# Kernel tuning notes

Hardware: AMD Instinct MI355X
Metric: run time of the kernel (lower is better)

The kernel has to match this reference:

```python
import jax, jax.numpy as jnp
import numpy as np

EPS = 1e-5

def _bn(x, gamma, beta):
    # BatchNorm1d in training mode: biased batch statistics over batch dim
    mu = jnp.mean(x, axis=0, keepdims=True)
    var = jnp.mean((x - mu) ** 2, axis=0, keepdims=True)
    return gamma * (x - mu) * jax.lax.rsqrt(var + EPS) + beta

def setup_inputs() -> dict:
    key = jax.random.key(0)
    ks = jax.random.split(key, 12)
    B, T, D_in, E, H, D_out = 8192, 128, 2, 128, 128, 5
    s = lambda k, shape, fan: jax.random.normal(k, shape, jnp.float32) * (1.0 / np.sqrt(fan))
    return {
        "inputs": jax.random.normal(ks[0], (B, T, D_in), jnp.float32),
        "W_emb": s(ks[1], (E, D_in), D_in),
        "b_emb": jnp.zeros((E,), jnp.float32),
        "gamma_emb": jnp.ones((E,), jnp.float32),
        "beta_emb": jnp.zeros((E,), jnp.float32),
        "W_ih": s(ks[2], (4 * H, E), E),
        "b_ih": jnp.zeros((4 * H,), jnp.float32),
        "W_hh": s(ks[3], (4 * H, H), H),
        "b_hh": jnp.zeros((4 * H,), jnp.float32),
        "W_out": s(ks[4], (D_out, H), H),
        "b_out": jnp.zeros((D_out,), jnp.float32),
        "gamma_out": jnp.ones((D_out,), jnp.float32),
        "beta_out": jnp.zeros((D_out,), jnp.float32),
    }

def reference(inputs, W_emb, b_emb, gamma_emb, beta_emb,
              W_ih, b_ih, W_hh, b_hh,
              W_out, b_out, gamma_out, beta_out):
    B, T, _ = inputs.shape
    H = W_hh.shape[1]
    x_t = jnp.swapaxes(inputs, 0, 1)  # [T, B, D_in]

    def step(carry, x):
        h, c = carry
        # input embedding MLP: Linear -> BatchNorm -> ReLU
        e = jax.nn.relu(_bn(x @ W_emb.T + b_emb, gamma_emb, beta_emb))
        # LSTMCell: gate order i, f, g, o (torch convention)
        gates = e @ W_ih.T + b_ih + h @ W_hh.T + b_hh
        i, f, g, o = jnp.split(gates, 4, axis=-1)
        c_new = jax.nn.sigmoid(f) * c + jax.nn.sigmoid(i) * jnp.tanh(g)
        h_new = jax.nn.sigmoid(o) * jnp.tanh(c_new)
        # output MLP: Linear -> BatchNorm (no activation)
        out = _bn(h_new @ W_out.T + b_out, gamma_out, beta_out)
        return (h_new, c_new), out

    init = (jnp.zeros((B, H), inputs.dtype), jnp.zeros((B, H), inputs.dtype))
    (h, c), outs = jax.lax.scan(step, init, x_t)
    return jnp.swapaxes(outs, 0, 1), (h, c)
```

## Files before the change

kernel.cpp:

```cpp
#include <hip/hip_runtime.h>

typedef short s16x8 __attribute__((ext_vector_type(8)));
typedef float f32x4 __attribute__((ext_vector_type(4)));

#define T_STEPS 128
#define BN_EPS 1e-5f

__device__ __forceinline__ unsigned short f2bf(float f) {
  unsigned u = __float_as_uint(f);
  u += 0x7FFFu + ((u >> 16) & 1u);
  return (unsigned short)(u >> 16);
}
__device__ __forceinline__ float sigm(float x) {
  return __builtin_amdgcn_rcpf(1.0f + __expf(-x));
}
__device__ __forceinline__ float tanh_(float x) {
  return 1.0f - 2.0f * __builtin_amdgcn_rcpf(1.0f + __expf(2.0f * x));
}

__global__ void moments_kernel(const float* __restrict__ inp, float* __restrict__ mom, int B) {
  int t = blockIdx.x;
  int tid = threadIdx.x;
  float s0 = 0.f, s1 = 0.f, q0 = 0.f, q1 = 0.f, pp = 0.f;
  for (int b = tid; b < B; b += 256) {
    float2 x = *(const float2*)(inp + (size_t)b * (2 * T_STEPS) + 2 * t);
    s0 += x.x; s1 += x.y; q0 += x.x * x.x; q1 += x.y * x.y; pp += x.x * x.y;
  }
  float v[5] = {s0, s1, q0, q1, pp};
  #pragma unroll
  for (int i = 0; i < 5; ++i) {
    float x = v[i];
    #pragma unroll
    for (int o = 32; o > 0; o >>= 1) x += __shfl_down(x, o);
    v[i] = x;
  }
  __shared__ float red[4][5];
  if ((tid & 63) == 0) {
    #pragma unroll
    for (int i = 0; i < 5; ++i) red[tid >> 6][i] = v[i];
  }
  __syncthreads();
  if (tid == 0) {
    #pragma unroll
    for (int i = 0; i < 5; ++i)
      mom[t * 5 + i] = red[0][i] + red[1][i] + red[2][i] + red[3][i];
  }
}

__global__ void fold_kernel(const float* __restrict__ mom,
                            const float* __restrict__ W_emb, const float* __restrict__ b_emb,
                            const float* __restrict__ gamma, const float* __restrict__ beta,
                            float* __restrict__ cA, float* __restrict__ cB, float* __restrict__ cC,
                            float invB) {
  int idx = blockIdx.x * 256 + threadIdx.x;
  if (idx >= T_STEPS * 128) return;
  int t = idx >> 7, j = idx & 127;
  float m0 = mom[t * 5 + 0] * invB, m1 = mom[t * 5 + 1] * invB;
  float q0 = mom[t * 5 + 2] * invB, q1 = mom[t * 5 + 3] * invB, p = mom[t * 5 + 4] * invB;
  float v00 = q0 - m0 * m0, v11 = q1 - m1 * m1, v01 = p - m0 * m1;
  float w0 = W_emb[2 * j], w1 = W_emb[2 * j + 1];
  float mu  = w0 * m0 + w1 * m1 + b_emb[j];
  float var = w0 * w0 * v00 + w1 * w1 * v11 + 2.f * w0 * w1 * v01;
  float a = gamma[j] * rsqrtf(var + BN_EPS);
  cA[idx] = a * w0;
  cB[idx] = a * w1;
  cC[idx] = beta[j] + a * (b_emb[j] - mu);
}

__global__ void prepw_kernel(const float* __restrict__ Wih, const float* __restrict__ Whh,
                             const float* __restrict__ Wout,
                             unsigned short* __restrict__ Wb, unsigned short* __restrict__ Wob) {
  int idx = blockIdx.x * 256 + threadIdx.x;
  if (idx < 512 * 256) {
    int n = idx >> 8, k = idx & 255;
    float w = (k < 128) ? Wih[n * 128 + k] : Whh[n * 128 + (k - 128)];
    Wb[idx] = f2bf(w);
  } else if (idx < 512 * 256 + 16 * 128) {
    int i2 = idx - 512 * 256;
    int d = i2 >> 7, k = i2 & 127;
    Wob[i2] = (d < 5) ? f2bf(Wout[d * 128 + k]) : (unsigned short)0;
  }
}

__global__ __launch_bounds__(512, 2) void lstm_kernel(
    const float* __restrict__ inp,
    const float* __restrict__ cA, const float* __restrict__ cB, const float* __restrict__ cC,
    const unsigned short* __restrict__ Wb, const unsigned short* __restrict__ Wob,
    const float* __restrict__ bih, const float* __restrict__ bhh,
    float* __restrict__ outz, float* __restrict__ hout, float* __restrict__ cout) {
  __shared__ __align__(16) short X[32][392];

  const int tid  = threadIdx.x;
  const int wave = tid >> 6;
  const int lane = tid & 63;
  const int l15  = lane & 15;
  const int lk   = lane >> 4;
  const int b0   = blockIdx.x * 32;
  const int em   = tid >> 4;
  const int ecg  = tid & 15;

  s16x8 wfrag[4][8];
  #pragma unroll
  for (int g = 0; g < 4; ++g)
    #pragma unroll
    for (int kk = 0; kk < 8; ++kk)
      wfrag[g][kk] = *(const s16x8*)(Wb + (size_t)(g * 128 + wave * 16 + l15) * 256 + kk * 32 + lk * 8);
  s16x8 wof[4];
  #pragma unroll
  for (int kk = 0; kk < 4; ++kk)
    wof[kk] = *(const s16x8*)(Wob + l15 * 128 + kk * 32 + lk * 8);
  float biasg[4];
  #pragma unroll
  for (int g = 0; g < 4; ++g) {
    int n = g * 128 + wave * 16 + l15;
    biasg[g] = bih[n] + bhh[n];
  }

  float creg[2][4] = {{0.f,0.f,0.f,0.f},{0.f,0.f,0.f,0.f}};
  float hreg[2][4] = {{0.f,0.f,0.f,0.f},{0.f,0.f,0.f,0.f}};

  auto do_e = [&](int tn) {
    float2 xv = *(const float2*)(inp + (size_t)(b0 + em) * (2 * T_STEPS) + 2 * tn);
    const float4* pa = (const float4*)(cA + tn * 128 + ecg * 8);
    const float4* pb = (const float4*)(cB + tn * 128 + ecg * 8);
    const float4* pc = (const float4*)(cC + tn * 128 + ecg * 8);
    s16x8 ev;
    #pragma unroll
    for (int q = 0; q < 2; ++q) {
      float4 va = pa[q], vb = pb[q], vc = pc[q];
      float e0 = fmaxf(0.f, vc.x + va.x * xv.x + vb.x * xv.y);
      float e1 = fmaxf(0.f, vc.y + va.y * xv.x + vb.y * xv.y);
      float e2 = fmaxf(0.f, vc.z + va.z * xv.x + vb.z * xv.y);
      float e3 = fmaxf(0.f, vc.w + va.w * xv.x + vb.w * xv.y);
      ev[4 * q + 0] = (short)f2bf(e0);
      ev[4 * q + 1] = (short)f2bf(e1);
      ev[4 * q + 2] = (short)f2bf(e2);
      ev[4 * q + 3] = (short)f2bf(e3);
    }
    *(s16x8*)&X[em][ecg * 8] = ev;
  };

  {
    s16x8 z = {0,0,0,0,0,0,0,0};
    *(s16x8*)&X[em][128 + ecg * 8] = z;
  }
  do_e(0);
  __syncthreads();

  #pragma unroll 1
  for (int t = 0; t < T_STEPS; ++t) {
    const int rb = 128 + (t & 1) * 128;
    const int wb = 128 + ((t + 1) & 1) * 128;
    f32x4 acc[2][4];
    #pragma unroll
    for (int mf = 0; mf < 2; ++mf)
      #pragma unroll
      for (int g = 0; g < 4; ++g) {
        f32x4 v = {biasg[g], biasg[g], biasg[g], biasg[g]};
        acc[mf][g] = v;
      }
    #pragma unroll
    for (int kk = 0; kk < 8; ++kk) {
      const int coff = (kk < 4) ? (kk * 32 + lk * 8) : (rb + (kk - 4) * 32 + lk * 8);
      s16x8 a0 = *(const s16x8*)&X[l15][coff];
      s16x8 a1 = *(const s16x8*)&X[16 + l15][coff];
      #pragma unroll
      for (int g = 0; g < 4; ++g) {
        acc[0][g] = __builtin_amdgcn_mfma_f32_16x16x32_bf16(a0, wfrag[g][kk], acc[0][g], 0, 0, 0);
        acc[1][g] = __builtin_amdgcn_mfma_f32_16x16x32_bf16(a1, wfrag[g][kk], acc[1][g], 0, 0, 0);
      }
    }
    #pragma unroll
    for (int mf = 0; mf < 2; ++mf)
      #pragma unroll
      for (int r = 0; r < 4; ++r) {
        float gi = sigm(acc[mf][0][r]);
        float gf = sigm(acc[mf][1][r]);
        float gg = tanh_(acc[mf][2][r]);
        float go = sigm(acc[mf][3][r]);
        float cc = gf * creg[mf][r] + gi * gg;
        creg[mf][r] = cc;
        float hh = go * tanh_(cc);
        hreg[mf][r] = hh;
        X[mf * 16 + lk * 4 + r][wb + wave * 16 + l15] = (short)f2bf(hh);
      }
    __syncthreads();
    if (wave < 2) {
      f32x4 zac = {0.f, 0.f, 0.f, 0.f};
      #pragma unroll
      for (int kk = 0; kk < 4; ++kk) {
        s16x8 a = *(const s16x8*)&X[wave * 16 + l15][wb + kk * 32 + lk * 8];
        zac = __builtin_amdgcn_mfma_f32_16x16x32_bf16(a, wof[kk], zac, 0, 0, 0);
      }
      if (l15 < 5) {
        #pragma unroll
        for (int r = 0; r < 4; ++r) {
          int m = wave * 16 + lk * 4 + r;
          outz[((size_t)(b0 + m) * T_STEPS + t) * 5 + l15] = zac[r];
        }
      }
    }
    if (t < T_STEPS - 1) do_e(t + 1);
    __syncthreads();
  }

  #pragma unroll
  for (int mf = 0; mf < 2; ++mf)
    #pragma unroll
    for (int r = 0; r < 4; ++r) {
      int m = mf * 16 + lk * 4 + r;
      size_t base = (size_t)(b0 + m) * 128 + wave * 16 + l15;
      hout[base] = hreg[mf][r];
      cout[base] = creg[mf][r];
    }
}

__global__ void stats_kernel(const float* __restrict__ z, float* __restrict__ stats,
                             const float* __restrict__ gamma, const float* __restrict__ beta, int B) {
  int grp = blockIdx.x;
  int d = grp % 5;
  int tid = threadIdx.x;
  float s = 0.f, q = 0.f;
  for (int b = tid; b < B; b += 256) {
    float v = z[(size_t)b * (T_STEPS * 5) + grp];
    s += v; q += v * v;
  }
  #pragma unroll
  for (int o = 32; o > 0; o >>= 1) { s += __shfl_down(s, o); q += __shfl_down(q, o); }
  __shared__ float rs[4], rq[4];
  if ((tid & 63) == 0) { rs[tid >> 6] = s; rq[tid >> 6] = q; }
  __syncthreads();
  if (tid == 0) {
    s = rs[0] + rs[1] + rs[2] + rs[3];
    q = rq[0] + rq[1] + rq[2] + rq[3];
    float mean = s / (float)B;
    float var  = q / (float)B - mean * mean;
    float sc = gamma[d] * rsqrtf(var + BN_EPS);
    stats[grp * 2 + 0] = sc;
    stats[grp * 2 + 1] = beta[d] - mean * sc;
  }
}

__global__ void norm_kernel(float* __restrict__ z, const float* __restrict__ stats, int n) {
  int i = blockIdx.x * 512 + threadIdx.x;
  if (i < n) {
    int grp = i % (T_STEPS * 5);
    float2 st = *(const float2*)(stats + grp * 2);
    z[i] = z[i] * st.x + st.y;
  }
}

extern "C" void kernel_launch(void* const* d_in, const int* in_sizes, int n_in,
                              void* d_out, int out_size, void* d_ws, size_t ws_size,
                              hipStream_t stream) {
  const float* inp    = (const float*)d_in[0];
  const float* W_emb  = (const float*)d_in[1];
  const float* b_emb  = (const float*)d_in[2];
  const float* g_emb  = (const float*)d_in[3];
  const float* be_emb = (const float*)d_in[4];
  const float* Wih    = (const float*)d_in[5];
  const float* bih    = (const float*)d_in[6];
  const float* Whh    = (const float*)d_in[7];
  const float* bhh    = (const float*)d_in[8];
  const float* Wout   = (const float*)d_in[9];
  const float* g_out  = (const float*)d_in[11];
  const float* be_out = (const float*)d_in[12];

  const int B = in_sizes[0] / (2 * T_STEPS);

  char* ws = (char*)d_ws;
  float*          mom   = (float*)(ws + 0);
  float*          cA    = (float*)(ws + 4096);
  float*          cB    = (float*)(ws + 69632);
  float*          cC    = (float*)(ws + 135168);
  unsigned short* Wb    = (unsigned short*)(ws + 200704);
  unsigned short* Wob   = (unsigned short*)(ws + 462848);
  float*          stats = (float*)(ws + 466944);

  float* outz = (float*)d_out;
  float* hout = outz + (size_t)B * T_STEPS * 5;
  float* cout = hout + (size_t)B * 128;

  moments_kernel<<<T_STEPS, 256, 0, stream>>>(inp, mom, B);
  fold_kernel<<<(T_STEPS * 128 + 255) / 256, 256, 0, stream>>>(mom, W_emb, b_emb, g_emb, be_emb,
                                                               cA, cB, cC, 1.0f / (float)B);
  prepw_kernel<<<(512 * 256 + 16 * 128 + 255) / 256, 256, 0, stream>>>(Wih, Whh, Wout, Wb, Wob);
  lstm_kernel<<<B / 32, 512, 0, stream>>>(inp, cA, cB, cC, Wb, Wob, bih, bhh, outz, hout, cout);
  stats_kernel<<<T_STEPS * 5, 256, 0, stream>>>(outz, stats, g_out, be_out, B);
  const int n = B * T_STEPS * 5;
  norm_kernel<<<(n + 511) / 512, 512, 0, stream>>>(outz, stats, n);
}
```

Baseline: 508.5 us.

## Split LSTM K-reduction across 16 waves and restructure BN prep/stat kernels

The LSTM kernel now uses 1024 threads per block and splits the gate GEMM's K dimension in half: one half of the waves covers the embedding part and the other the recurrent part. Partial sums are exchanged through a new LDS buffer, which halves per-wave weight registers and MFMA chain length. It also packs bf16 conversion with v_cvt_pk_bf16_f32, moves output weights into LDS, and fuses the moments and fold kernels. The output BN statistics are replaced by a vectorized atomic-sum kernel plus a float4 normalize. In exchange it adds an extra LDS round trip, a memset, and float atomics, which make the summation order nondeterministic.

```diff
diff --git a/kernel.cpp b/kernel.cpp
--- a/kernel.cpp
+++ b/kernel.cpp
@@ -5,12 +5,19 @@
 
 #define T_STEPS 128
 #define BN_EPS 1e-5f
+#define LROW 392
+#define EXS 36
 
 __device__ __forceinline__ unsigned short f2bf(float f) {
   unsigned u = __float_as_uint(f);
   u += 0x7FFFu + ((u >> 16) & 1u);
   return (unsigned short)(u >> 16);
 }
+__device__ __forceinline__ unsigned cvtpk(float a, float b) {
+  unsigned r;
+  asm("v_cvt_pk_bf16_f32 %0, %1, %2" : "=v"(r) : "v"(a), "v"(b));
+  return r;
+}
 __device__ __forceinline__ float sigm(float x) {
   return __builtin_amdgcn_rcpf(1.0f + __expf(-x));
 }
@@ -18,9 +25,12 @@
   return 1.0f - 2.0f * __builtin_amdgcn_rcpf(1.0f + __expf(2.0f * x));
 }
 
-__global__ void moments_kernel(const float* __restrict__ inp, float* __restrict__ mom, int B) {
-  int t = blockIdx.x;
-  int tid = threadIdx.x;
+__global__ void prep_e_kernel(const float* __restrict__ inp,
+                              const float* __restrict__ W_emb, const float* __restrict__ b_emb,
+                              const float* __restrict__ gamma, const float* __restrict__ beta,
+                              float* __restrict__ cA, float* __restrict__ cB, float* __restrict__ cC,
+                              int B, float invB) {
+  int t = blockIdx.x, tid = threadIdx.x;
   float s0 = 0.f, s1 = 0.f, q0 = 0.f, q1 = 0.f, pp = 0.f;
   for (int b = tid; b < B; b += 256) {
     float2 x = *(const float2*)(inp + (size_t)b * (2 * T_STEPS) + 2 * t);
@@ -35,6 +45,7 @@
     v[i] = x;
   }
   __shared__ float red[4][5];
+  __shared__ float tot[5];
   if ((tid & 63) == 0) {
     #pragma unroll
     for (int i = 0; i < 5; ++i) red[tid >> 6][i] = v[i];
@@ -42,29 +53,23 @@
   __syncthreads();
   if (tid == 0) {
     #pragma unroll
-    for (int i = 0; i < 5; ++i)
-      mom[t * 5 + i] = red[0][i] + red[1][i] + red[2][i] + red[3][i];
-  }
-}
-
-__global__ void fold_kernel(const float* __restrict__ mom,
-                            const float* __restrict__ W_emb, const float* __restrict__ b_emb,
-                            const float* __restrict__ gamma, const float* __restrict__ beta,
-                            float* __restrict__ cA, float* __restrict__ cB, float* __restrict__ cC,
-                            float invB) {
-  int idx = blockIdx.x * 256 + threadIdx.x;
-  if (idx >= T_STEPS * 128) return;
-  int t = idx >> 7, j = idx & 127;
-  float m0 = mom[t * 5 + 0] * invB, m1 = mom[t * 5 + 1] * invB;
-  float q0 = mom[t * 5 + 2] * invB, q1 = mom[t * 5 + 3] * invB, p = mom[t * 5 + 4] * invB;
-  float v00 = q0 - m0 * m0, v11 = q1 - m1 * m1, v01 = p - m0 * m1;
-  float w0 = W_emb[2 * j], w1 = W_emb[2 * j + 1];
-  float mu  = w0 * m0 + w1 * m1 + b_emb[j];
-  float var = w0 * w0 * v00 + w1 * w1 * v11 + 2.f * w0 * w1 * v01;
-  float a = gamma[j] * rsqrtf(var + BN_EPS);
-  cA[idx] = a * w0;
-  cB[idx] = a * w1;
-  cC[idx] = beta[j] + a * (b_emb[j] - mu);
+    for (int i = 0; i < 5; ++i) tot[i] = red[0][i] + red[1][i] + red[2][i] + red[3][i];
+  }
+  __syncthreads();
+  if (tid < 128) {
+    int j = tid;
+    float m0 = tot[0] * invB, m1 = tot[1] * invB;
+    float q0m = tot[2] * invB, q1m = tot[3] * invB, p = tot[4] * invB;
+    float v00 = q0m - m0 * m0, v11 = q1m - m1 * m1, v01 = p - m0 * m1;
+    float w0 = W_emb[2 * j], w1 = W_emb[2 * j + 1];
+    float mu  = w0 * m0 + w1 * m1 + b_emb[j];
+    float var = w0 * w0 * v00 + w1 * w1 * v11 + 2.f * w0 * w1 * v01;
+    float a = gamma[j] * rsqrtf(var + BN_EPS);
+    int idx = t * 128 + j;
+    cA[idx] = a * w0;
+    cB[idx] = a * w1;
+    cC[idx] = beta[j] + a * (b_emb[j] - mu);
+  }
 }
 
 __global__ void prepw_kernel(const float* __restrict__ Wih, const float* __restrict__ Whh,
@@ -82,172 +87,196 @@
   }
 }
 
-__global__ __launch_bounds__(512, 2) void lstm_kernel(
+__global__ __launch_bounds__(1024) void lstm_kernel(
     const float* __restrict__ inp,
     const float* __restrict__ cA, const float* __restrict__ cB, const float* __restrict__ cC,
     const unsigned short* __restrict__ Wb, const unsigned short* __restrict__ Wob,
     const float* __restrict__ bih, const float* __restrict__ bhh,
     float* __restrict__ outz, float* __restrict__ hout, float* __restrict__ cout) {
-  __shared__ __align__(16) short X[32][392];
+  __shared__ __align__(16) short X[32][LROW];
+  __shared__ __align__(16) unsigned short WO[16][136];
+  __shared__ __align__(16) float EX[8][4][16][EXS];
 
   const int tid  = threadIdx.x;
   const int wave = tid >> 6;
   const int lane = tid & 63;
   const int l15  = lane & 15;
   const int lk   = lane >> 4;
+  const int eh   = (wave >> 3);
+  const int cg   = wave & 7;
   const int b0   = blockIdx.x * 32;
-  const int em   = tid >> 4;
-  const int ecg  = tid & 15;
-
-  s16x8 wfrag[4][8];
+  const int em   = tid >> 5;
+  const int ec4  = (tid & 31) * 4;
+
+  s16x8 wfrag[4][4];
   #pragma unroll
   for (int g = 0; g < 4; ++g)
     #pragma unroll
-    for (int kk = 0; kk < 8; ++kk)
-      wfrag[g][kk] = *(const s16x8*)(Wb + (size_t)(g * 128 + wave * 16 + l15) * 256 + kk * 32 + lk * 8);
-  s16x8 wof[4];
-  #pragma unroll
-  for (int kk = 0; kk < 4; ++kk)
-    wof[kk] = *(const s16x8*)(Wob + l15 * 128 + kk * 32 + lk * 8);
+    for (int kk = 0; kk < 4; ++kk)
+      wfrag[g][kk] = *(const s16x8*)(Wb + (size_t)(g * 128 + cg * 16 + l15) * 256 + eh * 128 + kk * 32 + lk * 8);
   float biasg[4];
   #pragma unroll
   for (int g = 0; g < 4; ++g) {
-    int n = g * 128 + wave * 16 + l15;
-    biasg[g] = bih[n] + bhh[n];
-  }
-
-  float creg[2][4] = {{0.f,0.f,0.f,0.f},{0.f,0.f,0.f,0.f}};
-  float hreg[2][4] = {{0.f,0.f,0.f,0.f},{0.f,0.f,0.f,0.f}};
+    int n = g * 128 + cg * 16 + l15;
+    biasg[g] = eh ? 0.f : (bih[n] + bhh[n]);
+  }
+
+  {
+    int i0 = tid * 2;
+    int d = i0 >> 7, k = i0 & 127;
+    *(unsigned*)&WO[d][k] = *(const unsigned*)(Wob + i0);
+  }
 
   auto do_e = [&](int tn) {
     float2 xv = *(const float2*)(inp + (size_t)(b0 + em) * (2 * T_STEPS) + 2 * tn);
-    const float4* pa = (const float4*)(cA + tn * 128 + ecg * 8);
-    const float4* pb = (const float4*)(cB + tn * 128 + ecg * 8);
-    const float4* pc = (const float4*)(cC + tn * 128 + ecg * 8);
-    s16x8 ev;
-    #pragma unroll
-    for (int q = 0; q < 2; ++q) {
-      float4 va = pa[q], vb = pb[q], vc = pc[q];
-      float e0 = fmaxf(0.f, vc.x + va.x * xv.x + vb.x * xv.y);
-      float e1 = fmaxf(0.f, vc.y + va.y * xv.x + vb.y * xv.y);
-      float e2 = fmaxf(0.f, vc.z + va.z * xv.x + vb.z * xv.y);
-      float e3 = fmaxf(0.f, vc.w + va.w * xv.x + vb.w * xv.y);
-      ev[4 * q + 0] = (short)f2bf(e0);
-      ev[4 * q + 1] = (short)f2bf(e1);
-      ev[4 * q + 2] = (short)f2bf(e2);
-      ev[4 * q + 3] = (short)f2bf(e3);
-    }
-    *(s16x8*)&X[em][ecg * 8] = ev;
+    float4 va = *(const float4*)(cA + tn * 128 + ec4);
+    float4 vb = *(const float4*)(cB + tn * 128 + ec4);
+    float4 vc = *(const float4*)(cC + tn * 128 + ec4);
+    float e0 = fmaxf(0.f, vc.x + va.x * xv.x + vb.x * xv.y);
+    float e1 = fmaxf(0.f, vc.y + va.y * xv.x + vb.y * xv.y);
+    float e2 = fmaxf(0.f, vc.z + va.z * xv.x + vb.z * xv.y);
+    float e3 = fmaxf(0.f, vc.w + va.w * xv.x + vb.w * xv.y);
+    *(uint2*)&X[em][ec4] = make_uint2(cvtpk(e0, e1), cvtpk(e2, e3));
   };
 
-  {
-    s16x8 z = {0,0,0,0,0,0,0,0};
-    *(s16x8*)&X[em][128 + ecg * 8] = z;
-  }
+  *(uint2*)&X[em][128 + ec4] = make_uint2(0u, 0u);
   do_e(0);
   __syncthreads();
+
+  float creg[4] = {0.f, 0.f, 0.f, 0.f};
+  float hreg[4] = {0.f, 0.f, 0.f, 0.f};
+  const int colX    = cg * 16 + l15;
+  const int keep_r0 = eh ? 16 : 0;
+  const int rowP    = keep_r0 + lk * 4;
 
   #pragma unroll 1
   for (int t = 0; t < T_STEPS; ++t) {
     const int rb = 128 + (t & 1) * 128;
     const int wb = 128 + ((t + 1) & 1) * 128;
-    f32x4 acc[2][4];
-    #pragma unroll
-    for (int mf = 0; mf < 2; ++mf)
-      #pragma unroll
-      for (int g = 0; g < 4; ++g) {
-        f32x4 v = {biasg[g], biasg[g], biasg[g], biasg[g]};
-        acc[mf][g] = v;
-      }
-    #pragma unroll
-    for (int kk = 0; kk < 8; ++kk) {
-      const int coff = (kk < 4) ? (kk * 32 + lk * 8) : (rb + (kk - 4) * 32 + lk * 8);
+    const int abase = eh ? rb : 0;
+
+    f32x4 acc0[4], acc1[4];
+    #pragma unroll
+    for (int g = 0; g < 4; ++g) {
+      f32x4 v = {biasg[g], biasg[g], biasg[g], biasg[g]};
+      acc0[g] = v; acc1[g] = v;
+    }
+    #pragma unroll
+    for (int kk = 0; kk < 4; ++kk) {
+      const int coff = abase + kk * 32 + lk * 8;
       s16x8 a0 = *(const s16x8*)&X[l15][coff];
       s16x8 a1 = *(const s16x8*)&X[16 + l15][coff];
       #pragma unroll
       for (int g = 0; g < 4; ++g) {
-        acc[0][g] = __builtin_amdgcn_mfma_f32_16x16x32_bf16(a0, wfrag[g][kk], acc[0][g], 0, 0, 0);
-        acc[1][g] = __builtin_amdgcn_mfma_f32_16x16x32_bf16(a1, wfrag[g][kk], acc[1][g], 0, 0, 0);
+        acc0[g] = __builtin_amdgcn_mfma_f32_16x16x32_bf16(a0, wfrag[g][kk], acc0[g], 0, 0, 0);
+        acc1[g] = __builtin_amdgcn_mfma_f32_16x16x32_bf16(a1, wfrag[g][kk], acc1[g], 0, 0, 0);
       }
     }
-    #pragma unroll
-    for (int mf = 0; mf < 2; ++mf)
-      #pragma unroll
-      for (int r = 0; r < 4; ++r) {
-        float gi = sigm(acc[mf][0][r]);
-        float gf = sigm(acc[mf][1][r]);
-        float gg = tanh_(acc[mf][2][r]);
-        float go = sigm(acc[mf][3][r]);
-        float cc = gf * creg[mf][r] + gi * gg;
-        creg[mf][r] = cc;
-        float hh = go * tanh_(cc);
-        hreg[mf][r] = hh;
-        X[mf * 16 + lk * 4 + r][wb + wave * 16 + l15] = (short)f2bf(hh);
-      }
+    if (!eh) {
+      #pragma unroll
+      for (int g = 0; g < 4; ++g)
+        *(f32x4*)&EX[cg][g][l15][16 + lk * 4] = acc1[g];
+    } else {
+      #pragma unroll
+      for (int g = 0; g < 4; ++g)
+        *(f32x4*)&EX[cg][g][l15][lk * 4] = acc0[g];
+    }
     __syncthreads();
-    if (wave < 2) {
+    f32x4 gacc[4];
+    if (!eh) {
+      #pragma unroll
+      for (int g = 0; g < 4; ++g)
+        gacc[g] = acc0[g] + *(const f32x4*)&EX[cg][g][l15][lk * 4];
+    } else {
+      #pragma unroll
+      for (int g = 0; g < 4; ++g)
+        gacc[g] = acc1[g] + *(const f32x4*)&EX[cg][g][l15][16 + lk * 4];
+    }
+    float hv[4];
+    #pragma unroll
+    for (int r = 0; r < 4; ++r) {
+      float gi = sigm(gacc[0][r]);
+      float gf = sigm(gacc[1][r]);
+      float gg = tanh_(gacc[2][r]);
+      float go = sigm(gacc[3][r]);
+      float cc = gf * creg[r] + gi * gg;
+      creg[r] = cc;
+      float hh = go * tanh_(cc);
+      hreg[r] = hh; hv[r] = hh;
+    }
+    {
+      unsigned u01 = cvtpk(hv[0], hv[1]);
+      unsigned u23 = cvtpk(hv[2], hv[3]);
+      X[rowP + 0][wb + colX] = (short)(u01);
+      X[rowP + 1][wb + colX] = (short)(u01 >> 16);
+      X[rowP + 2][wb + colX] = (short)(u23);
+      X[rowP + 3][wb + colX] = (short)(u23 >> 16);
+    }
+    if (t < T_STEPS - 1) do_e(t + 1);
+    __syncthreads();
+    if ((wave & 7) == 0) {
+      const int rz = eh ? 16 : 0;
       f32x4 zac = {0.f, 0.f, 0.f, 0.f};
       #pragma unroll
       for (int kk = 0; kk < 4; ++kk) {
-        s16x8 a = *(const s16x8*)&X[wave * 16 + l15][wb + kk * 32 + lk * 8];
-        zac = __builtin_amdgcn_mfma_f32_16x16x32_bf16(a, wof[kk], zac, 0, 0, 0);
+        s16x8 a  = *(const s16x8*)&X[rz + l15][wb + kk * 32 + lk * 8];
+        s16x8 wz = *(const s16x8*)&WO[l15][kk * 32 + lk * 8];
+        zac = __builtin_amdgcn_mfma_f32_16x16x32_bf16(a, wz, zac, 0, 0, 0);
       }
       if (l15 < 5) {
         #pragma unroll
-        for (int r = 0; r < 4; ++r) {
-          int m = wave * 16 + lk * 4 + r;
-          outz[((size_t)(b0 + m) * T_STEPS + t) * 5 + l15] = zac[r];
-        }
+        for (int r = 0; r < 4; ++r)
+          outz[((size_t)(b0 + rz + lk * 4 + r) * T_STEPS + t) * 5 + l15] = zac[r];
       }
     }
-    if (t < T_STEPS - 1) do_e(t + 1);
-    __syncthreads();
-  }
-
-  #pragma unroll
-  for (int mf = 0; mf < 2; ++mf)
-    #pragma unroll
-    for (int r = 0; r < 4; ++r) {
-      int m = mf * 16 + lk * 4 + r;
-      size_t base = (size_t)(b0 + m) * 128 + wave * 16 + l15;
-      hout[base] = hreg[mf][r];
-      cout[base] = creg[mf][r];
-    }
-}
-
-__global__ void stats_kernel(const float* __restrict__ z, float* __restrict__ stats,
-                             const float* __restrict__ gamma, const float* __restrict__ beta, int B) {
-  int grp = blockIdx.x;
-  int d = grp % 5;
-  int tid = threadIdx.x;
-  float s = 0.f, q = 0.f;
-  for (int b = tid; b < B; b += 256) {
-    float v = z[(size_t)b * (T_STEPS * 5) + grp];
-    s += v; q += v * v;
-  }
-  #pragma unroll
-  for (int o = 32; o > 0; o >>= 1) { s += __shfl_down(s, o); q += __shfl_down(q, o); }
-  __shared__ float rs[4], rq[4];
-  if ((tid & 63) == 0) { rs[tid >> 6] = s; rq[tid >> 6] = q; }
-  __syncthreads();
-  if (tid == 0) {
-    s = rs[0] + rs[1] + rs[2] + rs[3];
-    q = rq[0] + rq[1] + rq[2] + rq[3];
-    float mean = s / (float)B;
-    float var  = q / (float)B - mean * mean;
+  }
+
+  #pragma unroll
+  for (int r = 0; r < 4; ++r) {
+    size_t base = (size_t)(b0 + rowP + r) * 128 + colX;
+    hout[base] = hreg[r];
+    cout[base] = creg[r];
+  }
+}
+
+__global__ void zsum_kernel(const float* __restrict__ z, float* __restrict__ st, int B) {
+  int g = blockIdx.x * 256 + threadIdx.x;
+  int c = g % 160, rg = g / 160;
+  float s[4] = {0.f, 0.f, 0.f, 0.f}, q[4] = {0.f, 0.f, 0.f, 0.f};
+  for (int b = rg; b < B; b += 256) {
+    float4 v = *(const float4*)(z + (size_t)b * 640 + c * 4);
+    s[0] += v.x; q[0] += v.x * v.x;
+    s[1] += v.y; q[1] += v.y * v.y;
+    s[2] += v.z; q[2] += v.z * v.z;
+    s[3] += v.w; q[3] += v.w * v.w;
+  }
+  #pragma unroll
+  for (int k = 0; k < 4; ++k) {
+    atomicAdd(&st[(c * 4 + k) * 2 + 0], s[k]);
+    atomicAdd(&st[(c * 4 + k) * 2 + 1], q[k]);
+  }
+}
+
+__global__ void norm_kernel(float* __restrict__ z, const float* __restrict__ st,
+                            const float* __restrict__ gamma, const float* __restrict__ beta,
+                            int n4, float invB) {
+  int i = blockIdx.x * 256 + threadIdx.x;
+  if (i >= n4) return;
+  int c = i % 160;
+  float4 v = *(const float4*)(z + (size_t)i * 4);
+  float o[4] = {v.x, v.y, v.z, v.w};
+  #pragma unroll
+  for (int k = 0; k < 4; ++k) {
+    int grp = c * 4 + k;
+    int d = grp % 5;
+    float S = st[grp * 2], Q = st[grp * 2 + 1];
+    float mean = S * invB;
+    float var  = Q * invB - mean * mean;
     float sc = gamma[d] * rsqrtf(var + BN_EPS);
-    stats[grp * 2 + 0] = sc;
-    stats[grp * 2 + 1] = beta[d] - mean * sc;
-  }
-}
-
-__global__ void norm_kernel(float* __restrict__ z, const float* __restrict__ stats, int n) {
-  int i = blockIdx.x * 512 + threadIdx.x;
-  if (i < n) {
-    int grp = i % (T_STEPS * 5);
-    float2 st = *(const float2*)(stats + grp * 2);
-    z[i] = z[i] * st.x + st.y;
-  }
+    o[k] = o[k] * sc + (beta[d] - mean * sc);
+  }
+  float4 w = {o[0], o[1], o[2], o[3]};
+  *(float4*)(z + (size_t)i * 4) = w;
 }
 
 extern "C" void kernel_launch(void* const* d_in, const int* in_sizes, int n_in,
@@ -269,24 +298,24 @@
   const int B = in_sizes[0] / (2 * T_STEPS);
 
   char* ws = (char*)d_ws;
-  float*          mom   = (float*)(ws + 0);
-  float*          cA    = (float*)(ws + 4096);
-  float*          cB    = (float*)(ws + 69632);
-  float*          cC    = (float*)(ws + 135168);
-  unsigned short* Wb    = (unsigned short*)(ws + 200704);
-  unsigned short* Wob   = (unsigned short*)(ws + 462848);
-  float*          stats = (float*)(ws + 466944);
+  float*          cAp = (float*)(ws + 0);
+  float*          cBp = (float*)(ws + 65536);
+  float*          cCp = (float*)(ws + 131072);
+  unsigned short* Wb  = (unsigned short*)(ws + 196608);
+  unsigned short* Wob = (unsigned short*)(ws + 458752);
+  float*          st  = (float*)(ws + 462848);
 
   float* outz = (float*)d_out;
   float* hout = outz + (size_t)B * T_STEPS * 5;
   float* cout = hout + (size_t)B * 128;
 
-  moments_kernel<<<T_STEPS, 256, 0, stream>>>(inp, mom, B);
-  fold_kernel<<<(T_STEPS * 128 + 255) / 256, 256, 0, stream>>>(mom, W_emb, b_emb, g_emb, be_emb,
-                                                               cA, cB, cC, 1.0f / (float)B);
+  const float invB = 1.0f / (float)B;
+
+  prep_e_kernel<<<T_STEPS, 256, 0, stream>>>(inp, W_emb, b_emb, g_emb, be_emb, cAp, cBp, cCp, B, invB);
   prepw_kernel<<<(512 * 256 + 16 * 128 + 255) / 256, 256, 0, stream>>>(Wih, Whh, Wout, Wb, Wob);
-  lstm_kernel<<<B / 32, 512, 0, stream>>>(inp, cA, cB, cC, Wb, Wob, bih, bhh, outz, hout, cout);
-  stats_kernel<<<T_STEPS * 5, 256, 0, stream>>>(outz, stats, g_out, be_out, B);
-  const int n = B * T_STEPS * 5;
-  norm_kernel<<<(n + 511) / 512, 512, 0, stream>>>(outz, stats, n);
-}
+  hipMemsetAsync(st, 0, 1280 * sizeof(float), stream);
+  lstm_kernel<<<B / 32, 1024, 0, stream>>>(inp, cAp, cBp, cCp, Wb, Wob, bih, bhh, outz, hout, cout);
+  zsum_kernel<<<160, 256, 0, stream>>>(outz, st, B);
+  const int n4 = B * (T_STEPS * 5) / 4;
+  norm_kernel<<<(n4 + 255) / 256, 256, 0, stream>>>(outz, st, g_out, be_out, n4, invB);
+}
```

New measurement: 709.9 us. +39.6%, slower.
